# Kernel optimization log

Hardware: AMD Instinct MI355X
Metric: run time of the kernel (lower is better)

## Reference

```python
import jax, jax.numpy as jnp
import numpy as np

PATCH = 3      # patch_size = (3, 3)
STRIDE = 1     # filter_patch_stride == compare_stride == 1
EPS = 1e-12    # F.normalize eps


def extract_patches(x, ph, pw, stride):
    """x: (B, C, H, W) -> (B, nH*nW, C, ph, pw), valid patches."""
    B, C, H, W = x.shape
    oh = (H - ph) // stride + 1
    ow = (W - pw) // stride + 1
    rows = (jnp.arange(oh) * stride)[:, None] + jnp.arange(ph)[None, :]  # (oh, ph)
    cols = (jnp.arange(ow) * stride)[:, None] + jnp.arange(pw)[None, :]  # (ow, pw)
    # gather -> (B, C, oh, ph, ow, pw)
    p = x[:, :, rows[:, :, None, None], cols[None, None, :, :]]
    return p.transpose(0, 2, 4, 1, 3, 5).reshape(B, oh * ow, C, ph, pw)


def l2norm(x, axis):
    # matches F.normalize(p=2): x / max(||x||, eps)
    return x / jnp.maximum(jnp.linalg.norm(x, axis=axis, keepdims=True), EPS)


def setup_inputs() -> dict:
    key = jax.random.key(0)
    k1, k2 = jax.random.split(key)
    pred_style = jax.random.normal(k1, (4, 256, 64, 64), dtype=jnp.float32)
    target_style = jax.random.normal(k2, (4, 256, 64, 64), dtype=jnp.float32)
    return {"pred_style": pred_style, "target_style": target_style}


def reference(pred_style, target_style):
    # patches of the raw (unnormalized) features
    tp = extract_patches(target_style, PATCH, PATCH, STRIDE)   # (B, nP, C, ph, pw)
    pp = extract_patches(pred_style, PATCH, PATCH, STRIDE)     # (B, nP, C, ph, pw)

    # best_match: normalize content feature over channels, style patches over channel dim (dim=2)
    x1n = l2norm(pred_style, axis=1)
    tpn = l2norm(tp, axis=2)
    x1p = extract_patches(x1n, PATCH, PATCH, STRIDE)           # (B, nP, C, ph, pw)

    # conv-as-cosine-correlation == batched patch dot products, then argmax over style patches
    scores = jnp.einsum('bqcij,bpcij->bqp', x1p, tpn)          # (B, nP, nP)
    match = jnp.argmax(scores, axis=2)                         # (B, nP)

    # gather best-matching target patches (indices detached in original via .data)
    new_t = jnp.take_along_axis(tp, match[:, :, None, None, None], axis=1)
    return jnp.mean((pp - new_t) ** 2)
```

## Files before the change

### kernel.cpp

```cpp
#include <hip/hip_runtime.h>
#include <hip/hip_bf16.h>

#define NB 4
#define CH 256
#define HH 64
#define WW 64
#define NPIX 4096
#define OH 62
#define NPATCH 3844
#define KDIM 256
#define EPSN 1e-12f
#define VROW 68
#define SEG 8
#define PST 68

typedef __attribute__((ext_vector_type(8))) short short8;
typedef __attribute__((ext_vector_type(4))) float f32x4;

__device__ __forceinline__ float bf16_to_f32(unsigned short u) {
    return __uint_as_float((unsigned)u << 16);
}
__device__ __forceinline__ unsigned short f32_to_bf16(float f) {
    __hip_bfloat16 h = __float2bfloat16(f);
    return *(unsigned short*)&h;
}

__global__ __launch_bounds__(256) void k_prep(const float* __restrict__ pred,
                                              const float* __restrict__ tgt,
                                              __hip_bfloat16* __restrict__ Xn,
                                              __hip_bfloat16* __restrict__ Tn,
                                              float* __restrict__ ssP, float* __restrict__ invP,
                                              float* __restrict__ ssT, float* __restrict__ invT,
                                              unsigned long long* __restrict__ keys,
                                              float* __restrict__ out) {
    const int bz = blockIdx.y;
    const int b = bz >> 1, which = bz & 1;
    const float* src = (which ? tgt : pred) + (size_t)b * CH * NPIX;
    unsigned short* dst = (unsigned short*)((which ? Tn : Xn) + (size_t)b * NPIX * CH);
    float* ss_g  = (which ? ssT  : ssP)  + b * NPIX;
    float* inv_g = (which ? invT : invP) + b * NPIX;
    const int pix0 = blockIdx.x * 64;
    const int t = threadIdx.x, lane = t & 63, wv = t >> 6;

    int gid = (bz * 64 + blockIdx.x) * 256 + t;
    if (gid < NB * NPATCH) keys[gid] = 0ull;
    if (gid == 0) out[0] = 0.f;

    __shared__ unsigned short stage[CH][PST];
    __shared__ float partial[16][68];
    __shared__ float inv_s[64];

    const int cb = t >> 4, chk = t & 15;
    float ss0 = 0.f, ss1 = 0.f, ss2 = 0.f, ss3 = 0.f;
#pragma unroll
    for (int r = 0; r < 16; ++r) {
        int c = cb * 16 + r;
        float4 v = *(const float4*)&src[(size_t)c * NPIX + pix0 + chk * 4];
        ss0 += v.x * v.x; ss1 += v.y * v.y; ss2 += v.z * v.z; ss3 += v.w * v.w;
        ushort4 sv;
        sv.x = f32_to_bf16(v.x); sv.y = f32_to_bf16(v.y);
        sv.z = f32_to_bf16(v.z); sv.w = f32_to_bf16(v.w);
        *(ushort4*)&stage[c][chk * 4] = sv;
    }
    float4 pv; pv.x = ss0; pv.y = ss1; pv.z = ss2; pv.w = ss3;
    *(float4*)&partial[cb][chk * 4] = pv;
    __syncthreads();
    if (t < 64) {
        float ss = 0.f;
#pragma unroll
        for (int r = 0; r < 16; ++r) ss += partial[r][t];
        float inv = 1.f / fmaxf(sqrtf(ss), EPSN);
        ss_g[pix0 + t] = ss;
        inv_g[pix0 + t] = inv;
        inv_s[t] = inv;
    }
    __syncthreads();
    for (int p = wv; p < 64; p += 4) {
        float iv = inv_s[p];
#pragma unroll
        for (int cc = 0; cc < 4; ++cc) {
            int c = cc * 64 + lane;
            float v = bf16_to_f32(stage[c][p]) * iv;
            dst[(size_t)(pix0 + p) * CH + c] = f32_to_bf16(v);
        }
    }
}

__device__ __forceinline__ void gload_lds16(const void* g, void* l) {
    __builtin_amdgcn_global_load_lds(
        (const __attribute__((address_space(1))) void*)g,
        (__attribute__((address_space(3))) void*)l, 16, 0, 0);
}

__global__ __launch_bounds__(256, 2) void k_gemm(const __hip_bfloat16* __restrict__ A,
                                                 const __hip_bfloat16* __restrict__ Bm,
                                                 unsigned short* __restrict__ Dout,
                                                 int zbase) {
    __shared__ __align__(16) short smem[32768];
#define ASOFF(buf) ((buf) * 8192)
#define BSOFF(buf) (16384 + (buf) * 8192)

    const int t = threadIdx.x;
    const int lane = t & 63, wv = t >> 6;
    const int wm = wv >> 1, wn = wv & 1;

    const int bid = ((blockIdx.z << 5) + blockIdx.y) * 32 + blockIdx.x;
    const int swz = ((bid & 7) << 8) + (bid >> 3);
    const int z = zbase + (swz >> 10), by = (swz >> 5) & 31, bx = swz & 31;

    const int row0 = by * 128, col0 = bx * 128;
    const short* Ag = (const short*)A + (size_t)z * NPIX * CH;
    const short* Bg = (const short*)Bm + (size_t)z * NPIX * CH;
    unsigned short* D = Dout + (size_t)z * NPIX * NPIX;

    const int srow = t >> 3;
    const int kce  = ((t & 7) ^ (srow & 7)) * 8;

    f32x4 acc[4][4] = {};

#define STAGE_K(buf, k0)                                                                   \
    do {                                                                                   \
        _Pragma("unroll")                                                                  \
        for (int rr_ = 0; rr_ < 4; ++rr_)                                                  \
            gload_lds16(Ag + (size_t)(row0 + rr_ * 32 + srow) * KDIM + (k0) + kce,         \
                        &smem[ASOFF(buf) + rr_ * 2048 + wv * 512]);                        \
        _Pragma("unroll")                                                                  \
        for (int rr_ = 0; rr_ < 4; ++rr_)                                                  \
            gload_lds16(Bg + (size_t)(col0 + rr_ * 32 + srow) * KDIM + (k0) + kce,         \
                        &smem[BSOFF(buf) + rr_ * 2048 + wv * 512]);                        \
    } while (0)

    const int rsel = lane & 15, kq = lane >> 4;
    const int rx = rsel & 7;

#define CONSUME(buf)                                                                       \
    do {                                                                                   \
        _Pragma("unroll")                                                                  \
        for (int s = 0; s < 2; ++s) {                                                      \
            const int pk = (((s << 2) + kq) ^ rx) * 8;                                     \
            short8 a_[4], b_[4];                                                           \
            _Pragma("unroll")                                                              \
            for (int mi = 0; mi < 4; ++mi)                                                 \
                a_[mi] = *(const short8*)&smem[ASOFF(buf) + (wm * 64 + mi * 16 + rsel) * 64 + pk]; \
            _Pragma("unroll")                                                              \
            for (int ni = 0; ni < 4; ++ni)                                                 \
                b_[ni] = *(const short8*)&smem[BSOFF(buf) + (wn * 64 + ni * 16 + rsel) * 64 + pk]; \
            _Pragma("unroll")                                                              \
            for (int mi = 0; mi < 4; ++mi)                                                 \
                _Pragma("unroll")                                                          \
                for (int ni = 0; ni < 4; ++ni)                                             \
                    acc[mi][ni] = __builtin_amdgcn_mfma_f32_16x16x32_bf16(a_[mi], b_[ni],  \
                                                                          acc[mi][ni], 0, 0, 0); \
        }                                                                                  \
    } while (0)

#define KITER(it, VMC)                                              \
    do {                                                            \
        asm volatile("s_waitcnt vmcnt(" #VMC ")" ::: "memory");     \
        __builtin_amdgcn_sched_barrier(0);                          \
        __builtin_amdgcn_s_barrier();                               \
        __builtin_amdgcn_sched_barrier(0);                          \
        CONSUME((it) & 1);                                          \
        asm volatile("s_waitcnt lgkmcnt(0)" ::: "memory");          \
        __builtin_amdgcn_sched_barrier(0);                          \
        __builtin_amdgcn_s_barrier();                               \
        __builtin_amdgcn_sched_barrier(0);                          \
        if ((it) < 2) STAGE_K((it) & 1, ((it) + 2) * 64);           \
    } while (0)

    STAGE_K(0, 0);
    STAGE_K(1, 64);
    KITER(0, 8);
    KITER(1, 8);
    KITER(2, 8);
    KITER(3, 0);
#undef KITER
#undef CONSUME
#undef STAGE_K

    const int rbase = (lane >> 4) * 4, cbase = lane & 15;
    unsigned short* Cs = (unsigned short*)smem;
#pragma unroll
    for (int mi = 0; mi < 4; ++mi)
#pragma unroll
        for (int ni = 0; ni < 4; ++ni) {
            int c = wn * 64 + ni * 16 + cbase;
#pragma unroll
            for (int r = 0; r < 4; ++r) {
                int row = wm * 64 + mi * 16 + rbase + r;
                int pc = (((c >> 3) ^ (row & 15)) * 8) + (c & 7);
                Cs[row * 128 + pc] = f32_to_bf16(acc[mi][ni][r]);
            }
        }
    __syncthreads();
#pragma unroll
    for (int rd = 0; rd < 8; ++rd) {
        int rr = rd * 16 + (t >> 4);
        int pc = ((t & 15) ^ (rr & 15)) * 8;
        uint4 v = *(const uint4*)&Cs[rr * 128 + pc];
        *(uint4*)&D[(size_t)(row0 + rr) * NPIX + col0 + (t & 15) * 8] = v;
    }
#undef ASOFF
#undef BSOFF
}

__device__ __forceinline__ void load_tile16(const unsigned short* __restrict__ D,
                                            int row, int col, float* f) {
    const unsigned short* rp = D + (size_t)row * NPIX + col;
    uint4 u0 = *(const uint4*)rp;
    uint4 u1 = *(const uint4*)(rp + 8);
    const unsigned* w0 = (const unsigned*)&u0;
    const unsigned* w1 = (const unsigned*)&u1;
#pragma unroll
    for (int w = 0; w < 4; ++w) {
        f[2 * w]         = bf16_to_f32((unsigned short)w0[w]);
        f[2 * w + 1]     = bf16_to_f32((unsigned short)(w0[w] >> 16));
        f[8 + 2 * w]     = bf16_to_f32((unsigned short)w1[w]);
        f[8 + 2 * w + 1] = bf16_to_f32((unsigned short)(w1[w] >> 16));
    }
}

__global__ __launch_bounds__(256) void k_score(const unsigned short* __restrict__ Dbase,
                                               unsigned long long* __restrict__ keys) {
    const int z = blockIdx.z;
    const unsigned short* D = Dbase + (size_t)z * NPIX * NPIX;
    const int t = threadIdx.x;

    const int d = (int)blockIdx.x - 61;
    const int adg = d < 0 ? -d : d;
    const int len = 62 - adg;
    const int s0 = blockIdx.y * SEG;
    if (s0 >= len) return;
    const int steps = min(SEG, len - s0);
    const int qr0 = (d > 0 ? d : 0) + s0;
    const int pr0 = qr0 - d;

    __shared__ __align__(16) float V[64 * VROW];

    const int a = t >> 2, b0 = (t & 3) * 16;
    const int g = t >> 6, qc = t & 63;
    const int qcr = qc < OH ? qc : (OH - 1);
    const int pc0 = g * 16;
    const int kmax = (g == 3) ? 14 : 16;

    float A[16], B[16], C[16];
    load_tile16(D, (qr0 + 0) * 64 + a, (pr0 + 0) * 64 + b0, A);
    load_tile16(D, (qr0 + 1) * 64 + a, (pr0 + 1) * 64 + b0, B);

    for (int k = 0; k < steps; ++k) {
        load_tile16(D, (qr0 + k + 2) * 64 + a, (pr0 + k + 2) * 64 + b0, C);
        float v[16];
#pragma unroll
        for (int e = 0; e < 16; ++e) v[e] = A[e] + B[e] + C[e];
        if (k) __syncthreads();
#pragma unroll
        for (int e = 0; e < 16; e += 4)
            *(f32x4*)&V[a * VROW + b0 + e] = *(const f32x4*)&v[e];
        __syncthreads();

        float r0[16], r1[20], r2[20];
#pragma unroll
        for (int e = 0; e < 16; e += 4)
            *(f32x4*)&r0[e] = *(const f32x4*)&V[qcr * VROW + pc0 + e];
#pragma unroll
        for (int e = 0; e < 20; e += 4)
            *(f32x4*)&r1[e] = *(const f32x4*)&V[(qcr + 1) * VROW + pc0 + e];
#pragma unroll
        for (int e = 0; e < 20; e += 4)
            *(f32x4*)&r2[e] = *(const f32x4*)&V[(qcr + 2) * VROW + pc0 + e];
        float best = -1e30f; int bpc = 0;
#pragma unroll
        for (int kk = 0; kk < 16; ++kk) {
            float s = r0[kk] + r1[kk + 1] + r2[kk + 2];
            if (kk < kmax && s > best) { best = s; bpc = pc0 + kk; }
        }
        if (qc < OH) {
            unsigned u = __float_as_uint(best);
            u = (best >= 0.f) ? (u | 0x80000000u) : ~u;
            unsigned long long key = ((unsigned long long)u << 12)
                                   | (unsigned)((63 - (pr0 + k)) << 6)
                                   | (unsigned)(63 - bpc);
            atomicMax(&keys[(size_t)z * NPATCH + (qr0 + k) * OH + qc], key);
        }
#pragma unroll
        for (int e = 0; e < 16; ++e) { A[e] = B[e]; B[e] = C[e]; }
    }
}

__global__ void k_loss(const unsigned short* __restrict__ Dbase,
                       const unsigned long long* __restrict__ keys,
                       const float* __restrict__ ssPb, const float* __restrict__ invPb,
                       const float* __restrict__ ssTb, const float* __restrict__ invTb,
                       float* __restrict__ out) {
    const int z = blockIdx.y;
    const unsigned short* D = Dbase + (size_t)z * NPIX * NPIX;
    const float* ssP  = ssPb  + z * NPIX;
    const float* invP = invPb + z * NPIX;
    const float* ssT  = ssTb  + z * NPIX;
    const float* invT = invTb + z * NPIX;
    int q = blockIdx.x * 256 + threadIdx.x;
    float acc = 0.f;
    if (q < NPATCH) {
        int qr = q / OH, qc = q - qr * OH;
        int qpix = qr * WW + qc;
        unsigned long long key = keys[(size_t)z * NPATCH + q];
        int mpr = 63 - (int)((key >> 6) & 63);
        int mpc = 63 - (int)(key & 63);
        int mpix = mpr * WW + mpc;
#pragma unroll
        for (int i = 0; i < 3; ++i)
#pragma unroll
            for (int j = 0; j < 3; ++j) {
                int off = i * WW + j;
                int y = qpix + off, x = mpix + off;
                float Dv = bf16_to_f32(D[(size_t)y * NPIX + x]);
                float nP = ssP[y] * invP[y];
                float nT = ssT[x] * invT[x];
                acc += ssP[y] + ssT[x] - 2.f * Dv * nP * nT;
            }
    }
#pragma unroll
    for (int s = 32; s > 0; s >>= 1) acc += __shfl_down(acc, s, 64);
    if ((threadIdx.x & 63) == 0)
        atomicAdd(out, acc * (1.f / 35426304.f));
}

extern "C" void kernel_launch(void* const* d_in, const int* in_sizes, int n_in,
                              void* d_out, int out_size, void* d_ws, size_t ws_size,
                              hipStream_t stream) {
    const float* pred = (const float*)d_in[0];
    const float* tgt  = (const float*)d_in[1];
    char* ws = (char*)d_ws;
    unsigned short*     Dws  = (unsigned short*)(ws);
    __hip_bfloat16*     Xn   = (__hip_bfloat16*)(ws + 134217728);
    __hip_bfloat16*     Tn   = (__hip_bfloat16*)(ws + 142606336);
    float*              ssP  = (float*)(ws + 150994944);
    float*              invP = (float*)(ws + 151060480);
    float*              ssT  = (float*)(ws + 151126016);
    float*              invT = (float*)(ws + 151191552);
    unsigned long long* keys = (unsigned long long*)(ws + 151257088);

    k_prep<<<dim3(64, 8), 256, 0, stream>>>(pred, tgt, Xn, Tn, ssP, invP, ssT, invT,
                                            keys, (float*)d_out);
    k_gemm<<<dim3(32, 32, 2), 256, 0, stream>>>(Xn, Tn, Dws, 0);
    k_gemm<<<dim3(32, 32, 2), 256, 0, stream>>>(Xn, Tn, Dws, 2);
    k_score<<<dim3(123, 8, 4), 256, 0, stream>>>(Dws, keys);
    k_loss<<<dim3(16, 4), 256, 0, stream>>>(Dws, keys, ssP, invP, ssT, invT,
                                            (float*)d_out);
}
```

Measured before the change: 181.8 us.

## Compute 3x3 diagonal patch sums in registers with shuffle argmax instead of LDS

The scoring kernel no longer stages per-step vertical sums in shared memory. Each thread now loads three consecutive rows of the pixel-dot matrix (18 columns each) and forms the full 3x3 diagonal sum directly in registers. The argmax across the four column groups is reduced with wave shuffles, and the three register buffers are rotated through an unrolled macro. This removes LDS traffic and both __syncthreads per step, at the cost of roughly three times more global (mostly cache-hitting) loads per step and higher register pressure.

Result: no change. 179.9 us (-1.1%).

```diff
diff --git a/kernel.cpp b/kernel.cpp
--- a/kernel.cpp
+++ b/kernel.cpp
@@ -10,7 +10,6 @@
 #define NPATCH 3844
 #define KDIM 256
 #define EPSN 1e-12f
-#define VROW 68
 #define SEG 8
 #define PST 68
 
@@ -204,20 +203,35 @@
 #undef BSOFF
 }
 
-__device__ __forceinline__ void load_tile16(const unsigned short* __restrict__ D,
-                                            int row, int col, float* f) {
-    const unsigned short* rp = D + (size_t)row * NPIX + col;
+__device__ __forceinline__ void load_row18(const unsigned short* __restrict__ rp,
+                                           bool full, float* o) {
     uint4 u0 = *(const uint4*)rp;
     uint4 u1 = *(const uint4*)(rp + 8);
+    unsigned e = full ? *(const unsigned*)(rp + 16) : 0u;
     const unsigned* w0 = (const unsigned*)&u0;
     const unsigned* w1 = (const unsigned*)&u1;
 #pragma unroll
     for (int w = 0; w < 4; ++w) {
-        f[2 * w]         = bf16_to_f32((unsigned short)w0[w]);
-        f[2 * w + 1]     = bf16_to_f32((unsigned short)(w0[w] >> 16));
-        f[8 + 2 * w]     = bf16_to_f32((unsigned short)w1[w]);
-        f[8 + 2 * w + 1] = bf16_to_f32((unsigned short)(w1[w] >> 16));
-    }
+        o[2 * w]         = bf16_to_f32((unsigned short)w0[w]);
+        o[2 * w + 1]     = bf16_to_f32((unsigned short)(w0[w] >> 16));
+        o[8 + 2 * w]     = bf16_to_f32((unsigned short)w1[w]);
+        o[8 + 2 * w + 1] = bf16_to_f32((unsigned short)(w1[w] >> 16));
+    }
+    o[16] = bf16_to_f32((unsigned short)e);
+    o[17] = bf16_to_f32((unsigned short)(e >> 16));
+}
+
+__device__ __forceinline__ void gtile(const unsigned short* __restrict__ D,
+                                      int tr, int tc, int a, int b0, bool full,
+                                      float* G) {
+    const unsigned short* base = D + (size_t)(tr * 64 + a) * NPIX + tc * 64 + b0;
+    float r0[18], r1[18], r2[18];
+    load_row18(base, full, r0);
+    load_row18(base + NPIX, full, r1);
+    load_row18(base + 2 * NPIX, full, r2);
+#pragma unroll
+    for (int kk = 0; kk < 16; ++kk)
+        G[kk] = r0[kk] + r1[kk + 1] + r2[kk + 2];
 }
 
 __global__ __launch_bounds__(256) void k_score(const unsigned short* __restrict__ Dbase,
@@ -235,56 +249,52 @@
     const int qr0 = (d > 0 ? d : 0) + s0;
     const int pr0 = qr0 - d;
 
-    __shared__ __align__(16) float V[64 * VROW];
-
-    const int a = t >> 2, b0 = (t & 3) * 16;
-    const int g = t >> 6, qc = t & 63;
-    const int qcr = qc < OH ? qc : (OH - 1);
-    const int pc0 = g * 16;
-    const int kmax = (g == 3) ? 14 : 16;
-
-    float A[16], B[16], C[16];
-    load_tile16(D, (qr0 + 0) * 64 + a, (pr0 + 0) * 64 + b0, A);
-    load_tile16(D, (qr0 + 1) * 64 + a, (pr0 + 1) * 64 + b0, B);
-
-    for (int k = 0; k < steps; ++k) {
-        load_tile16(D, (qr0 + k + 2) * 64 + a, (pr0 + k + 2) * 64 + b0, C);
-        float v[16];
-#pragma unroll
-        for (int e = 0; e < 16; ++e) v[e] = A[e] + B[e] + C[e];
-        if (k) __syncthreads();
-#pragma unroll
-        for (int e = 0; e < 16; e += 4)
-            *(f32x4*)&V[a * VROW + b0 + e] = *(const f32x4*)&v[e];
-        __syncthreads();
-
-        float r0[16], r1[20], r2[20];
-#pragma unroll
-        for (int e = 0; e < 16; e += 4)
-            *(f32x4*)&r0[e] = *(const f32x4*)&V[qcr * VROW + pc0 + e];
-#pragma unroll
-        for (int e = 0; e < 20; e += 4)
-            *(f32x4*)&r1[e] = *(const f32x4*)&V[(qcr + 1) * VROW + pc0 + e];
-#pragma unroll
-        for (int e = 0; e < 20; e += 4)
-            *(f32x4*)&r2[e] = *(const f32x4*)&V[(qcr + 2) * VROW + pc0 + e];
-        float best = -1e30f; int bpc = 0;
-#pragma unroll
-        for (int kk = 0; kk < 16; ++kk) {
-            float s = r0[kk] + r1[kk + 1] + r2[kk + 2];
-            if (kk < kmax && s > best) { best = s; bpc = pc0 + kk; }
-        }
-        if (qc < OH) {
-            unsigned u = __float_as_uint(best);
-            u = (best >= 0.f) ? (u | 0x80000000u) : ~u;
-            unsigned long long key = ((unsigned long long)u << 12)
-                                   | (unsigned)((63 - (pr0 + k)) << 6)
-                                   | (unsigned)(63 - bpc);
-            atomicMax(&keys[(size_t)z * NPATCH + (qr0 + k) * OH + qc], key);
-        }
-#pragma unroll
-        for (int e = 0; e < 16; ++e) { A[e] = B[e]; B[e] = C[e]; }
-    }
+    const int a = t >> 2;
+    const int gcol = t & 3;
+    const int b0 = gcol * 16;
+    const int kmax = (gcol == 3) ? 14 : 16;
+    const bool full = (gcol < 3);
+    const bool act = (a < OH);
+
+    float G0[16], G1[16], G2[16];
+    if (act) {
+        gtile(D, qr0 + 0, pr0 + 0, a, b0, full, G0);
+        gtile(D, qr0 + 1, pr0 + 1, a, b0, full, G1);
+    }
+
+#define SCORE_STEP(K, GA, GB, GC)                                                 \
+    if ((K) < steps) {                                                            \
+        if (act) gtile(D, qr0 + (K) + 2, pr0 + (K) + 2, a, b0, full, GC);         \
+        float best = -1e30f; int bpc = 0;                                         \
+        _Pragma("unroll")                                                         \
+        for (int kk = 0; kk < 16; ++kk) {                                         \
+            float s = GA[kk] + GB[kk] + GC[kk];                                   \
+            if (kk < kmax && s > best) { best = s; bpc = b0 + kk; }               \
+        }                                                                         \
+        float os_; int opc_;                                                      \
+        os_ = __shfl_xor(best, 1, 64); opc_ = __shfl_xor(bpc, 1, 64);             \
+        if (os_ > best || (os_ == best && opc_ < bpc)) { best = os_; bpc = opc_; }\
+        os_ = __shfl_xor(best, 2, 64); opc_ = __shfl_xor(bpc, 2, 64);             \
+        if (os_ > best || (os_ == best && opc_ < bpc)) { best = os_; bpc = opc_; }\
+        if (act && gcol == 0) {                                                   \
+            unsigned u = __float_as_uint(best);                                   \
+            u = (best >= 0.f) ? (u | 0x80000000u) : ~u;                           \
+            unsigned long long key = ((unsigned long long)u << 12)                \
+                                   | (unsigned)((63 - (pr0 + (K))) << 6)          \
+                                   | (unsigned)(63 - bpc);                        \
+            atomicMax(&keys[(size_t)z * NPATCH + (qr0 + (K)) * OH + a], key);     \
+        }                                                                         \
+    }
+
+    SCORE_STEP(0, G0, G1, G2)
+    SCORE_STEP(1, G1, G2, G0)
+    SCORE_STEP(2, G2, G0, G1)
+    SCORE_STEP(3, G0, G1, G2)
+    SCORE_STEP(4, G1, G2, G0)
+    SCORE_STEP(5, G2, G0, G1)
+    SCORE_STEP(6, G0, G1, G2)
+    SCORE_STEP(7, G1, G2, G0)
+#undef SCORE_STEP
 }
 
 __global__ void k_loss(const unsigned short* __restrict__ Dbase,
```
